# Kernel optimization log

Hardware: AMD Instinct MI355X
Metric: run time of the kernel (lower is better)

## Reference

```python
import jax, jax.numpy as jnp
import numpy as np
from jax import lax

B, DIM, H, W = 32, 64, 1, 8192
HEADS = 8
EPS_LN = 1e-5
EPS_NORM = 1e-12


def setup_inputs() -> dict:
    key = jax.random.key(0)
    ks = jax.random.split(key, 20)
    g = lambda i, shape, s=0.05: jax.random.normal(ks[i], shape, jnp.float32) * s
    return dict(
        x=jax.random.normal(ks[0], (B, DIM, H, W), jnp.float32),
        qkv_w=g(1, (3 * DIM, DIM)), qkv_b=g(2, (3 * DIM,)),
        dw_w=g(3, (3 * DIM, 1, 3, 3)), dw_b=g(4, (3 * DIM,)),
        proj_w=g(5, (DIM, DIM)), proj_b=g(6, (DIM,)),
        temperature=jnp.ones((HEADS, 1, 1), jnp.float32),
        sp_w=g(7, (DIM,)), sp_b=g(8, (1,)),
        up_w=g(9, (3,)), up_b=g(10, (3,)),
        c2_w=g(11, (1, 1, 2)), c2_b=g(11, (1,)), ln2_w=jnp.ones((W,), jnp.float32), ln2_b=jnp.zeros((W,), jnp.float32),
        c4_w=g(12, (1, 1, 4)), c4_b=g(13, (1,)), ln4_w=jnp.ones((W,), jnp.float32), ln4_b=jnp.zeros((W,), jnp.float32),
        c6_w=g(14, (1, 1, 6)), c6_b=g(15, (1,)), ln6_w=jnp.ones((W,), jnp.float32), ln6_b=jnp.zeros((W,), jnp.float32),
        mp_w=g(16, (DIM,)), mp_b=g(17, (DIM,)),
    )


def _mtl(xs, cw, cb, lw, lb):
    """Multiscale_Temporal_Layer: conv1d 'same' -> LayerNorm(W) -> ELU -> mean pool. xs: (b,1,w)."""
    k = cw.shape[-1]
    tot = k - 1
    lo = tot // 2  # torch 'same': extra pad goes to the right
    y = lax.conv_general_dilated(xs, cw, (1,), [(lo, tot - lo)],
                                 dimension_numbers=('NCH', 'OIH', 'NCH'))
    y = y + cb[None, :, None]
    mu = jnp.mean(y, -1, keepdims=True)
    var = jnp.mean((y - mu) ** 2, -1, keepdims=True)
    y = (y - mu) / jnp.sqrt(var + EPS_LN) * lw + lb
    y = jax.nn.elu(y)
    return jnp.mean(y, -1, keepdims=True)  # (b,1,1)


def _forward(x, qkv_w, qkv_b, dw_w, dw_b, proj_w, proj_b, temperature,
             sp_w, sp_b, up_w, up_b,
             c2_w, c2_b, ln2_w, ln2_b,
             c4_w, c4_b, ln4_w, ln4_b,
             c6_w, c6_b, ln6_w, ln6_b,
             mp_w, mp_b):
    b, c, h, w = x.shape
    hd = c // HEADS  # per-head channel dim
    # 1x1 conv qkv, then depthwise 3x3 conv
    qkv = jnp.einsum('oc,bchw->bohw', qkv_w, x) + qkv_b[None, :, None, None]
    qkv = lax.conv_general_dilated(qkv, dw_w, (1, 1), [(1, 1), (1, 1)],
                                   dimension_numbers=('NCHW', 'OIHW', 'NCHW'),
                                   feature_group_count=3 * c)
    qkv = qkv + dw_b[None, :, None, None]
    q, k, v = jnp.split(qkv, 3, axis=1)
    # Multiscale_Temporal_Attention on v: v is (b,c,1,w)
    xseq = (jnp.einsum('c,bcw->bw', sp_w, v[:, :, 0, :]) + sp_b)[:, None, :]  # (b,1,w)
    up = up_w[None, :, None] * xseq + up_b[None, :, None]  # (b,3,w)
    xx, yy, zz = up[:, 0:1], up[:, 1:2], up[:, 2:3]
    mout = (_mtl(xx, c2_w, c2_b, ln2_w, ln2_b) * xx
            + _mtl(yy, c4_w, c4_b, ln4_w, ln4_b) * yy
            + _mtl(zz, c6_w, c6_b, ln6_w, ln6_b) * zz)  # (b,1,w)
    v = mp_w[None, :, None] * mout + mp_b[None, :, None]  # (b,c,w) via 1x1 conv broadcast
    # channel (transposed) attention over n = h*w tokens
    n = h * w
    q = q.reshape(b, HEADS, hd, n)
    k = k.reshape(b, HEADS, hd, n)
    v = v.reshape(b, HEADS, hd, n)
    q = q / jnp.maximum(jnp.linalg.norm(q, axis=-1, keepdims=True), EPS_NORM)
    k = k / jnp.maximum(jnp.linalg.norm(k, axis=-1, keepdims=True), EPS_NORM)
    attn = jnp.einsum('bhcn,bhdn->bhcd', q, k) * temperature  # (b,heads,hd,hd)
    attn = jax.nn.softmax(attn, axis=-1)
    out = jnp.einsum('bhcd,bhdn->bhcn', attn, v).reshape(b, c, h, w)
    out = jnp.einsum('oc,bchw->bohw', proj_w, out) + proj_b[None, :, None, None]
    return out  # dropouts are identity in eval mode


def reference(x, qkv_w, qkv_b, dw_w, dw_b, proj_w, proj_b, temperature,
              sp_w, sp_b, up_w, up_b,
              c2_w, c2_b, ln2_w, ln2_b,
              c4_w, c4_b, ln4_w, ln4_b,
              c6_w, c6_b, ln6_w, ln6_b,
              mp_w, mp_b):
    return _forward(x, qkv_w, qkv_b, dw_w, dw_b, proj_w, proj_b, temperature,
                    sp_w, sp_b, up_w, up_b,
                    c2_w, c2_b, ln2_w, ln2_b,
                    c4_w, c4_b, ln4_w, ln4_b,
                    c6_w, c6_b, ln6_w, ln6_b,
                    mp_w, mp_b)
```

## Files before the change

### kernel.cpp

```cpp
#include <hip/hip_runtime.h>
#include <hip/hip_bf16.h>
#include <math.h>

#define Wd 8192
#define Bd 32

#define OFF_G    0
#define OFF_H    192
#define OFF_BASE 195
#define OFF_XSEQ 256
#define OFF_SXP  (OFF_XSEQ + Bd*Wd)
#define OFF_RX   (OFF_SXP + Bd*8*64)
#define OFF_T    (OFF_RX + Bd*8*12288)
#define OFF_VEC  (OFF_T + Bd*3*1152)
#define OFF_WM   (OFF_VEC + Bd*640)

typedef __attribute__((ext_vector_type(8))) short bf16x8;
typedef __attribute__((ext_vector_type(4))) float f32x4;

__device__ __forceinline__ unsigned short f2bf(float v) {
    return __builtin_bit_cast(unsigned short, __float2bfloat16(v));
}
__device__ __forceinline__ float bf2f(unsigned short h) {
    return __builtin_bit_cast(float, (unsigned)h << 16);
}

__global__ __launch_bounds__(256) void k0_setup(const float* __restrict__ qkv_w,
                         const float* __restrict__ qkv_b,
                         const float* __restrict__ dw_w, const float* __restrict__ dw_b,
                         const float* __restrict__ sp_w, const float* __restrict__ sp_b,
                         float* __restrict__ ws)
{
    __shared__ float sw[64*64];
    __shared__ float sdw[192];
    __shared__ float ssp[64], sqb[64], sdb[64];
    int tid = threadIdx.x;
    for (int i = tid; i < 4096; i += 256) sw[i] = qkv_w[128*64 + i];
    if (tid < 192) { int c = tid/3, j = tid - 3*c; sdw[tid] = dw_w[(128+c)*9 + 3 + j]; }
    if (tid < 64)  { ssp[tid] = sp_w[tid]; sqb[tid] = qkv_b[128+tid]; sdb[tid] = dw_b[128+tid]; }
    __syncthreads();
    if (tid < 192) {
        int j = tid >> 6, ch = tid & 63;
        float acc = 0.f;
        #pragma unroll 8
        for (int c = 0; c < 64; c++)
            acc += ssp[c] * sdw[c*3+j] * sw[c*64 + ch];
        ws[OFF_G + j*64 + ch] = acc;
    } else if (tid < 195) {
        int j = tid - 192;
        float h = 0.f;
        #pragma unroll 8
        for (int c = 0; c < 64; c++)
            h += ssp[c] * sdw[c*3+j] * sqb[c];
        ws[OFF_H + j] = h;
    } else if (tid == 195) {
        float base = sp_b[0];
        #pragma unroll 8
        for (int c = 0; c < 64; c++) base += ssp[c] * sdb[c];
        ws[OFF_BASE] = base;
    }
}

#define XSTR 152
#define XBYTES (64*XSTR*2)

__device__ __forceinline__ void loadpf(const float* __restrict__ xr, int wstart,
                                       int q, float4 pf[9]) {
    #pragma unroll
    for (int m = 0; m < 9; m++) {
        int gp = wstart - 8 + 36*q + 4*m;
        if (gp >= 0 && gp < Wd) pf[m] = *(const float4*)(xr + gp);
        else pf[m] = (float4){0.f,0.f,0.f,0.f};
    }
}
__device__ __forceinline__ float writepf(unsigned char* buf, int row, int q,
                                         const float4 pf[9]) {
    float ss = 0.f;
    #pragma unroll
    for (int m = 0; m < 9; m++) {
        int col0 = 36*q + 4*m;
        unsigned short h0 = f2bf(pf[m].x), h1 = f2bf(pf[m].y),
                       h2 = f2bf(pf[m].z), h3 = f2bf(pf[m].w);
        uint2 wv;
        wv.x = (unsigned)h0 | ((unsigned)h1 << 16);
        wv.y = (unsigned)h2 | ((unsigned)h3 << 16);
        *(uint2*)(buf + row*304 + col0*2) = wv;
        if (col0 >= 8 && col0 < 136)
            ss += (bf2f(h0) + bf2f(h1)) + (bf2f(h2) + bf2f(h3));
    }
    return ss;
}

__global__ __launch_bounds__(256) void kR(const float* __restrict__ x,
                                          float* __restrict__ ws)
{
    __shared__ __align__(16) unsigned char xb0[XBYTES];
    __shared__ __align__(16) unsigned char xb1[XBYTES];
    __shared__ float4 Gl[64];
    __shared__ float phib[3][132];
    __shared__ float sxb[64][4];

    const int tid = threadIdx.x, lane = tid & 63, wv = tid >> 6;
    const int g = lane >> 4, lr = lane & 15;
    const int chunk = blockIdx.x, b = blockIdx.y;
    const int w0 = chunk << 10;
    const int row = tid & 63, q = tid >> 6;
    const float* xr = x + ((size_t)b*64 + row)*Wd;

    if (tid < 64) Gl[tid] = (float4){ws[OFF_G+tid], ws[OFF_G+64+tid], ws[OFF_G+128+tid], 0.f};
    const float Hs0 = ws[OFF_H], Hs1 = ws[OFF_H+1], Hs2 = ws[OFF_H+2];
    const float base_ = ws[OFF_BASE];

    f32x4 a0[4], a1[4], a2[4];
    #pragma unroll
    for (int ct = 0; ct < 4; ct++) {
        a0[ct] = (f32x4){0,0,0,0}; a1[ct] = (f32x4){0,0,0,0}; a2[ct] = (f32x4){0,0,0,0};
    }
    float ssum = 0.f;
    float4 pf[9];

    loadpf(xr, w0, q, pf);
    ssum += writepf(xb0, row, q, pf);
    __syncthreads();

    for (int st = 0; st < 8; ++st) {
        const int p0 = w0 + (st << 7);
        unsigned char* bufc = (st & 1) ? xb1 : xb0;
        unsigned char* bufn = (st & 1) ? xb0 : xb1;

        if (st < 7) loadpf(xr, p0 + 128, q, pf);

        #pragma unroll
        for (int k = 0; k < 4; k++) {
            const unsigned char* ap = bufc + (16*wv + lr)*304 + 16 + 64*k + 16*g;
            bf16x8 A = *(const bf16x8*)ap;
            #pragma unroll
            for (int ct = 0; ct < 4; ct++) {
                const unsigned char* bp = bufc + (16*ct + lr)*304 + 16 + 64*k + 16*g;
                uint4 u = *(const uint4*)bp;
                unsigned u4 = *(const unsigned*)(bp + 16);
                uint4 v1 = { (u.x>>16)|(u.y<<16), (u.y>>16)|(u.z<<16),
                             (u.z>>16)|(u.w<<16), (u.w>>16)|(u4<<16) };
                uint4 v2 = { u.y, u.z, u.w, u4 };
                a0[ct] = __builtin_amdgcn_mfma_f32_16x16x32_bf16(A, __builtin_bit_cast(bf16x8,u),  a0[ct],0,0,0);
                a1[ct] = __builtin_amdgcn_mfma_f32_16x16x32_bf16(A, __builtin_bit_cast(bf16x8,v1), a1[ct],0,0,0);
                a2[ct] = __builtin_amdgcn_mfma_f32_16x16x32_bf16(A, __builtin_bit_cast(bf16x8,v2), a2[ct],0,0,0);
            }
        }
        if (tid < 130) {
            const unsigned short* xs = (const unsigned short*)bufc;
            float f0=0.f, f1=0.f, f2=0.f;
            int colw = 7 + tid;
            #pragma unroll 8
            for (int c = 0; c < 64; c++) {
                float xv = bf2f(xs[c*XSTR + colw]);
                float4 gv = Gl[c];
                f0 += gv.x*xv; f1 += gv.y*xv; f2 += gv.z*xv;
            }
            phib[0][tid]=f0; phib[1][tid]=f1; phib[2][tid]=f2;
        }
        __syncthreads();
        if (tid < 128) {
            int w = p0 + tid;
            float v = base_ + Hs0 + Hs1 + Hs2
                    + phib[0][tid] + phib[1][tid+1] + phib[2][tid+2];
            if (w == 0) v -= Hs0;
            if (w == Wd-1) v -= Hs2;
            ws[OFF_XSEQ + (size_t)b*Wd + w] = v;
        }
        if (st < 7) ssum += writepf(bufn, row, q, pf);
        __syncthreads();
    }

    {
        float* pb = ws + OFF_RX + (size_t)(b*8 + chunk)*12288;
        #pragma unroll
        for (int ct = 0; ct < 4; ct++) {
            #pragma unroll
            for (int r = 0; r < 4; r++) {
                int c = 16*wv + 4*g + r, cc = 16*ct + lr;
                pb[         c*64 + cc] = a0[ct][r];
                pb[4096  +  c*64 + cc] = a1[ct][r];
                pb[8192  +  c*64 + cc] = a2[ct][r];
            }
        }
    }
    sxb[row][q] = ssum;
    __syncthreads();
    if (tid < 64)
        ws[OFF_SXP + (size_t)(b*8 + chunk)*64 + tid] =
            (sxb[tid][0] + sxb[tid][1]) + (sxb[tid][2] + sxb[tid][3]);
}

#define KF_SW 0
#define KF_RX (128*68*4)
#define KF_NT (KF_RX + 64*68*4)
#define KF_SXR (KF_NT + 64*68*4)
#define KF_XC (KF_SXR + 64*4)
#define KF_BYTES (KF_XC + 256*4)

__device__ __forceinline__ float dot64p(const float* a, const float* b) {
    float s0=0.f,s1=0.f,s2=0.f,s3=0.f;
    #pragma unroll
    for (int k = 0; k < 64; k += 4) {
        float4 av = *(const float4*)(a+k), bv = *(const float4*)(b+k);
        s0 += av.x*bv.x; s1 += av.y*bv.y; s2 += av.z*bv.z; s3 += av.w*bv.w;
    }
    return (s0+s1)+(s2+s3);
}
__device__ __forceinline__ float blk_reduce_256(float v, float* sc) {
    #pragma unroll
    for (int off = 32; off > 0; off >>= 1) v += __shfl_down(v, off, 64);
    __syncthreads();
    if ((threadIdx.x & 63) == 0) sc[threadIdx.x >> 6] = v;
    __syncthreads();
    return sc[0] + sc[1] + sc[2] + sc[3];
}

__global__ __launch_bounds__(256) void kF(const float* __restrict__ x,
    const float* __restrict__ qkv_w,
    const float* __restrict__ up_w, const float* __restrict__ up_b,
    const float* __restrict__ c2_w, const float* __restrict__ c2_b,
    const float* __restrict__ ln2_w, const float* __restrict__ ln2_b,
    const float* __restrict__ c4_w, const float* __restrict__ c4_b,
    const float* __restrict__ ln4_w, const float* __restrict__ ln4_b,
    const float* __restrict__ c6_w, const float* __restrict__ c6_b,
    const float* __restrict__ ln6_w, const float* __restrict__ ln6_b,
    float* __restrict__ ws)
{
    __shared__ __align__(16) unsigned char sm[KF_BYTES];
    __shared__ float sc[4];
    const int tid = threadIdx.x, bx = blockIdx.x;

    if (bx < 96) {
        const int bb = bx / 3, d = bx - 3*bb;
        float* sW  = (float*)(sm + KF_SW);
        float* sRx = (float*)(sm + KF_RX);
        float* sNT = (float*)(sm + KF_NT);
        float* sxr = (float*)(sm + KF_SXR);
        float* xcol = (float*)(sm + KF_XC);

        #pragma unroll
        for (int k = 0; k < 8; k++) {
            int i4 = tid + 256*k;
            float4 v = ((const float4*)qkv_w)[i4];
            int r = i4 >> 4, c = (i4 & 15) << 2;
            *(float4*)(sW + r*68 + c) = v;
        }
        const float* rxp = ws + OFF_RX + (size_t)bb*8*12288 + d*4096;
        #pragma unroll
        for (int k = 0; k < 16; k++) {
            int idx = tid + 256*k;
            float s = 0.f;
            #pragma unroll
            for (int ch = 0; ch < 8; ch++) s += rxp[(size_t)ch*12288 + idx];
            sRx[(idx>>6)*68 + (idx&63)] = s;
        }
        if (d == 0) {
            if (tid < 64) {
                float s = 0.f;
                #pragma unroll
                for (int ch = 0; ch < 8; ch++) s += ws[OFF_SXP + (size_t)(bb*8+ch)*64 + tid];
                sxr[tid] = s;
            }
            {
                int c = tid & 63, v = tid >> 6;
                int colv = (v == 0) ? 0 : (v == 1) ? 1 : (v == 2) ? (Wd-2) : (Wd-1);
                xcol[v*64 + c] = x[((size_t)bb*64 + c)*Wd + colv];
            }
        }
        __syncthreads();
        if (d == 0 && tid < 128) {
            int r = tid;
            float Xi=0.f,x0=0.f,x1=0.f,xm2=0.f,xm1=0.f;
            #pragma unroll 8
            for (int c = 0; c < 64; c++) {
                float w = sW[r*68+c];
                Xi += w*sxr[c]; x0 += w*xcol[c]; x1 += w*xcol[64+c];
                xm2 += w*xcol[128+c]; xm1 += w*xcol[192+c];
            }
            float* vp = ws + OFF_VEC + bb*640;
            vp[r] = Xi; vp[128+r] = x0; vp[256+r] = x1; vp[384+r] = xm2; vp[512+r] = xm1;
        }
        {
            int ro = tid >> 4, co = tid & 15;
            float acc[4][4] = {};
            for (int k = 0; k < 64; k += 4) {
                float4 av[4], bv[4];
                #pragma unroll
                for (int i = 0; i < 4; i++) av[i] = *(const float4*)(sRx + (4*ro+i)*68 + k);
                #pragma unroll
                for (int j = 0; j < 4; j++) bv[j] = *(const float4*)(sW + (64+4*co+j)*68 + k);
                #pragma unroll
                for (int i = 0; i < 4; i++)
                    #pragma unroll
                    for (int j = 0; j < 4; j++)
                        acc[i][j] += av[i].x*bv[j].x + av[i].y*bv[j].y
                                   + av[i].z*bv[j].z + av[i].w*bv[j].w;
            }
            __syncthreads();
            #pragma unroll
            for (int i = 0; i < 4; i++)
                #pragma unroll
                for (int j = 0; j < 4; j++)
                    sNT[(4*co+j)*68 + 4*ro+i] = acc[i][j];
        }
        __syncthreads();
        float* Tp = ws + OFF_T + (size_t)(bb*3 + d)*1152;
        for (int e = tid; e < 512; e += 256) {
            int t = e >> 3, u = ((e>>6)<<3) + (e&7);
            Tp[e] = dot64p(sW + t*68, sNT + u*68);
        }
        if (tid < 64) Tp[1088 + tid] = dot64p(sW + (64+tid)*68, sNT + tid*68);
        __syncthreads();
        {
            int ro = tid >> 4, co = tid & 15;
            float acc[4][4] = {};
            for (int k = 0; k < 64; k += 4) {
                float4 av[4], bv[4];
                #pragma unroll
                for (int i = 0; i < 4; i++) av[i] = *(const float4*)(sRx + (4*ro+i)*68 + k);
                #pragma unroll
                for (int j = 0; j < 4; j++) bv[j] = *(const float4*)(sW + (4*co+j)*68 + k);
                #pragma unroll
                for (int i = 0; i < 4; i++)
                    #pragma unroll
                    for (int j = 0; j < 4; j++)
                        acc[i][j] += av[i].x*bv[j].x + av[i].y*bv[j].y
                                   + av[i].z*bv[j].z + av[i].w*bv[j].w;
            }
            __syncthreads();
            #pragma unroll
            for (int i = 0; i < 4; i++)
                #pragma unroll
                for (int j = 0; j < 4; j++)
                    sNT[(4*co+j)*68 + 4*ro+i] = acc[i][j];
        }
        __syncthreads();
        for (int e = tid; e < 512; e += 256) {
            int t = e >> 3, u = ((e>>6)<<3) + (e&7);
            Tp[512 + e] = dot64p(sW + (64+u)*68, sNT + t*68);
        }
        if (tid < 64) Tp[1024 + tid] = dot64p(sW + tid*68, sNT + tid*68);
        return;
    }

    int t2 = bx - 96;
    int br = t2 >> 5, b = t2 & 31;
    float* ys = (float*)sm;
    const float *cw, *lw, *lb; float cb; int K, lo;
    if (br == 0)      { cw = c2_w; cb = c2_b[0]; lw = ln2_w; lb = ln2_b; K = 2; lo = 0; }
    else if (br == 1) { cw = c4_w; cb = c4_b[0]; lw = ln4_w; lb = ln4_b; K = 4; lo = 1; }
    else              { cw = c6_w; cb = c6_b[0]; lw = ln6_w; lb = ln6_b; K = 6; lo = 2; }
    float uw = up_w[br], ub = up_b[br];
    const float* xr = ws + OFF_XSEQ + (size_t)b*Wd;

    float s = 0.f, s2 = 0.f;
    for (int w = tid; w < Wd; w += 256) {
        float y = cb;
        for (int m = 0; m < K; m++) {
            int p = w + m - lo;
            if (p >= 0 && p < Wd) y += cw[m] * (uw*xr[p] + ub);
        }
        ys[w] = y; s += y; s2 += y*y;
    }
    float mu = blk_reduce_256(s, sc) * (1.f/Wd);
    __syncthreads();
    float Ey2 = blk_reduce_256(s2, sc) * (1.f/Wd);
    float var = fmaxf(Ey2 - mu*mu, 0.f);
    float inv = 1.f / sqrtf(var + 1e-5f);
    float se = 0.f;
    for (int w = tid; w < Wd; w += 256) {
        float tt = (ys[w]-mu)*inv*lw[w] + lb[w];
        se += (tt > 0.f) ? tt : expm1f(tt);
    }
    float m = blk_reduce_256(se, sc) * (1.f/Wd);
    if (tid == 0) ws[OFF_WM + b*3 + br] = m;
}

__global__ __launch_bounds__(256) void k5_out(const float* __restrict__ ws,
    const float* __restrict__ qkv_b, const float* __restrict__ dw_w,
    const float* __restrict__ dw_b, const float* __restrict__ temperature,
    const float* __restrict__ mp_w, const float* __restrict__ mp_b,
    const float* __restrict__ up_w, const float* __restrict__ up_b,
    const float* __restrict__ proj_w, const float* __restrict__ proj_b,
    float* __restrict__ out)
{
    __shared__ float sT3[3][1152];
    __shared__ float vec[5][128];
    __shared__ float qb_[128], tb_[128], tp_[128][3];
    __shared__ float Sq[512], dgq[64], dgk[64];
    __shared__ float snk[64], sal[64], sbe[64], sE[64], sF[64];
    __shared__ float red[64][8];
    const int tid = threadIdx.x;
    const int chunk = blockIdx.x, b = blockIdx.y;

    for (int i = tid; i < 3456; i += 256) ((float*)sT3)[i] = ws[OFF_T + (size_t)b*3456 + i];
    for (int i = tid; i < 640; i += 256) ((float*)vec)[i] = ws[OFF_VEC + b*640 + i];
    if (tid < 128) {
        qb_[tid] = qkv_b[tid]; tb_[tid] = dw_b[tid];
        tp_[tid][0] = dw_w[tid*9+3]; tp_[tid][1] = dw_w[tid*9+4]; tp_[tid][2] = dw_w[tid*9+5];
    }
    __syncthreads();

    for (int ee = tid; ee < 640; ee += 256) {
        int r, s; float Tpv[3], Tmv[3];
        if (ee < 512) {
            r = ee >> 3; s = 64 + ((ee>>6)<<3) + (ee&7);
            #pragma unroll
            for (int d = 0; d < 3; d++) { Tpv[d] = sT3[d][ee]; Tmv[d] = sT3[d][512+ee]; }
        } else if (ee < 576) {
            r = s = ee - 512;
            #pragma unroll
            for (int d = 0; d < 3; d++) { Tpv[d] = Tmv[d] = sT3[d][1024 + r]; }
        } else {
            int u = ee - 576; r = s = 64 + u;
            #pragma unroll
            for (int d = 0; d < 3; d++) { Tpv[d] = Tmv[d] = sT3[d][1088 + u]; }
        }
        float Xr = vec[0][r], Xs = vec[0][s];
        float x0r = vec[1][r], x0s = vec[1][s];
        float x1r = vec[2][r], x1s = vec[2][s];
        float xm2r = vec[3][r], xm2s = vec[3][s];
        float xm1r = vec[4][r], xm1s = vec[4][s];
        float qr = qb_[r], qs = qb_[s];
        float C5[5];
        #pragma unroll
        for (int dd = 0; dd < 3; dd++) {
            float head_s = (dd>=1 ? x0s : 0.f) + (dd>=2 ? x1s : 0.f);
            float tail_r = (dd>=1 ? xm1r : 0.f) + (dd>=2 ? xm2r : 0.f);
            C5[2+dd] = Tpv[dd] + qr*(Xs - head_s) + qs*(Xr - tail_r) + (8192.f - dd)*qr*qs;
            float head_r = (dd>=1 ? x0r : 0.f) + (dd>=2 ? x1r : 0.f);
            float tail_s = (dd>=1 ? xm1s : 0.f) + (dd>=2 ? xm2s : 0.f);
            C5[2-dd] = Tmv[dd] + qs*(Xr - head_r) + qr*(Xs - tail_s) + (8192.f - dd)*qr*qs;
        }
        float y0r = x0r + qr, y0s = x0s + qs;
        float ym1r = xm1r + qr, ym1s = xm1s + qs;
        float Yr = Xr + 8192.f*qr, Ys = Xs + 8192.f*qs;
        float tbr = tb_[r], tbs = tb_[s];
        float G = 8192.f * tbr * tbs;
        float sumr = 0.f, sums = 0.f;
        #pragma unroll
        for (int i = 0; i < 3; i++) {
            sumr += tp_[r][i] * (Yr - (i==0 ? ym1r : 0.f) - (i==2 ? y0r : 0.f));
            sums += tp_[s][i] * (Ys - (i==0 ? ym1s : 0.f) - (i==2 ? y0s : 0.f));
        }
        G += tbr * sums + tbs * sumr;
        #pragma unroll
        for (int i = 0; i < 3; i++)
            #pragma unroll
            for (int j = 0; j < 3; j++) {
                float P = C5[2 + j - i];
                if (i == 2 && j == 2) P -= y0r * y0s;
                if (i == 0 && j == 0) P -= ym1r * ym1s;
                G += tp_[r][i] * tp_[s][j] * P;
            }
        if (ee < 512) Sq[ee] = G;
        else if (ee < 576) dgq[ee-512] = G;
        else dgk[ee-576] = G;
    }
    __syncthreads();

    float nq = 0.f;
    if (tid < 64) {
        nq = fmaxf(sqrtf(fmaxf(dgq[tid], 0.f)), 1e-12f);
        snk[tid] = fmaxf(sqrtf(fmaxf(dgk[tid], 0.f)), 1e-12f);
    }
    __syncthreads();
    if (tid < 64) {
        int h = tid >> 3;
        float temp = temperature[h];
        float lg[8], mx = -1e30f;
        #pragma unroll
        for (int d = 0; d < 8; d++) {
            lg[d] = Sq[tid*8 + d] / (nq * snk[h*8 + d]) * temp;
            mx = fmaxf(mx, lg[d]);
        }
        float sum = 0.f;
        #pragma unroll
        for (int d = 0; d < 8; d++) { lg[d] = expf(lg[d] - mx); sum += lg[d]; }
        float a = 0.f, bb2 = 0.f;
        #pragma unroll
        for (int d = 0; d < 8; d++) {
            float at = lg[d] / sum;
            a   += at * mp_w[h*8 + d];
            bb2 += at * mp_b[h*8 + d];
        }
        sal[tid] = a; sbe[tid] = bb2;
    }
    __syncthreads();
    {
        float m2 = ws[OFF_WM + b*3], m4 = ws[OFF_WM + b*3 + 1], m6 = ws[OFF_WM + b*3 + 2];
        float A_ = m2*up_w[0] + m4*up_w[1] + m6*up_w[2];
        float C_ = m2*up_b[0] + m4*up_b[1] + m6*up_b[2];
        int o = tid & 63, q = tid >> 6;
        float pa = 0.f, pb2 = 0.f;
        #pragma unroll
        for (int k = 0; k < 16; k++) {
            int c = 16*q + k;
            float pw = proj_w[o*64 + c];
            pa += pw * sal[c]; pb2 += pw * sbe[c];
        }
        red[o][q] = pa; red[o][4+q] = pb2;
        __syncthreads();
        if (tid < 64) {
            float Pa = (red[tid][0]+red[tid][1]) + (red[tid][2]+red[tid][3]);
            float Pb = (red[tid][4]+red[tid][5]) + (red[tid][6]+red[tid][7]);
            sE[tid] = A_ * Pa;
            sF[tid] = C_ * Pa + Pb + proj_b[tid];
        }
    }
    __syncthreads();
    const float4* xs4 = (const float4*)(ws + OFF_XSEQ + (size_t)b*Wd);
    float4 xv = xs4[chunk*128 + (tid & 127)];
    int oh = tid >> 7;
    float4* ob = (float4*)out + (size_t)b*64*2048 + chunk*128 + (tid & 127);
    #pragma unroll 8
    for (int oo = 0; oo < 32; oo++) {
        int o = oh*32 + oo;
        float e = sE[o], f = sF[o];
        float4 rr = { e*xv.x + f, e*xv.y + f, e*xv.z + f, e*xv.w + f };
        ob[(size_t)o*2048] = rr;
    }
}

extern "C" void kernel_launch(void* const* d_in, const int* in_sizes, int n_in,
                              void* d_out, int out_size, void* d_ws, size_t ws_size,
                              hipStream_t stream) {
    const float* x      = (const float*)d_in[0];
    const float* qkv_w  = (const float*)d_in[1];
    const float* qkv_b  = (const float*)d_in[2];
    const float* dw_w   = (const float*)d_in[3];
    const float* dw_b   = (const float*)d_in[4];
    const float* proj_w = (const float*)d_in[5];
    const float* proj_b = (const float*)d_in[6];
    const float* temperature = (const float*)d_in[7];
    const float* sp_w   = (const float*)d_in[8];
    const float* sp_b   = (const float*)d_in[9];
    const float* up_w   = (const float*)d_in[10];
    const float* up_b   = (const float*)d_in[11];
    const float* c2_w   = (const float*)d_in[12];
    const float* c2_b   = (const float*)d_in[13];
    const float* ln2_w  = (const float*)d_in[14];
    const float* ln2_b  = (const float*)d_in[15];
    const float* c4_w   = (const float*)d_in[16];
    const float* c4_b   = (const float*)d_in[17];
    const float* ln4_w  = (const float*)d_in[18];
    const float* ln4_b  = (const float*)d_in[19];
    const float* c6_w   = (const float*)d_in[20];
    const float* c6_b   = (const float*)d_in[21];
    const float* ln6_w  = (const float*)d_in[22];
    const float* ln6_b  = (const float*)d_in[23];
    const float* mp_w   = (const float*)d_in[24];
    const float* mp_b   = (const float*)d_in[25];
    float* ws  = (float*)d_ws;
    float* out = (float*)d_out;

    k0_setup<<<1, 256, 0, stream>>>(qkv_w, qkv_b, dw_w, dw_b, sp_w, sp_b, ws);
    kR<<<dim3(8, 32), 256, 0, stream>>>(x, ws);
    kF<<<192, 256, 0, stream>>>(x, qkv_w, up_w, up_b,
        c2_w, c2_b, ln2_w, ln2_b, c4_w, c4_b, ln4_w, ln4_b, c6_w, c6_b, ln6_w, ln6_b,
        ws);
    k5_out<<<dim3(16, 32), 256, 0, stream>>>(ws, qkv_b, dw_w, dw_b, temperature,
        mp_w, mp_b, up_w, up_b, proj_w, proj_b, out);
}
```

Baseline: 129.1 us.

## Split kR into 16 chunks with wider swizzled LDS tiles and coalesced loads

```diff
diff --git a/kernel.cpp b/kernel.cpp
--- a/kernel.cpp
+++ b/kernel.cpp
@@ -4,14 +4,15 @@
 
 #define Wd 8192
 #define Bd 32
+#define NCH 16
 
 #define OFF_G    0
 #define OFF_H    192
 #define OFF_BASE 195
 #define OFF_XSEQ 256
 #define OFF_SXP  (OFF_XSEQ + Bd*Wd)
-#define OFF_RX   (OFF_SXP + Bd*8*64)
-#define OFF_T    (OFF_RX + Bd*8*12288)
+#define OFF_RX   (OFF_SXP + Bd*NCH*64)
+#define OFF_T    (OFF_RX + Bd*NCH*12288)
 #define OFF_VEC  (OFF_T + Bd*3*1152)
 #define OFF_WM   (OFF_VEC + Bd*640)
 
@@ -61,51 +62,57 @@
     }
 }
 
-#define XSTR 152
-#define XBYTES (64*XSTR*2)
-
-__device__ __forceinline__ void loadpf(const float* __restrict__ xr, int wstart,
-                                       int q, float4 pf[9]) {
+#define ROWB 576
+
+__device__ __forceinline__ int swzoff(int row, int gr) {
+    int s = (gr < 32) ? (gr ^ (row & 7)) : gr;
+    return row*ROWB + s*16;
+}
+
+__device__ __forceinline__ void loadsub(const float* __restrict__ xbase, int p0,
+                                        float4 pf[17]) {
     #pragma unroll
-    for (int m = 0; m < 9; m++) {
-        int gp = wstart - 8 + 36*q + 4*m;
-        if (gp >= 0 && gp < Wd) pf[m] = *(const float4*)(xr + gp);
-        else pf[m] = (float4){0.f,0.f,0.f,0.f};
-    }
-}
-__device__ __forceinline__ float writepf(unsigned char* buf, int row, int q,
-                                         const float4 pf[9]) {
-    float ss = 0.f;
+    for (int m = 0; m < 17; m++) {
+        int F = threadIdx.x + 256*m;
+        int row = F / 68, c4 = F - 68*row;
+        int p = p0 - 8 + 4*c4;
+        const float* src = xbase + (size_t)row*Wd + p;
+        if ((unsigned)p <= (unsigned)(Wd-4)) {
+            pf[m] = *(const float4*)src;
+        } else {
+            float4 v;
+            v.x = ((unsigned)(p  ) < (unsigned)Wd) ? src[0] : 0.f;
+            v.y = ((unsigned)(p+1) < (unsigned)Wd) ? src[1] : 0.f;
+            v.z = ((unsigned)(p+2) < (unsigned)Wd) ? src[2] : 0.f;
+            v.w = ((unsigned)(p+3) < (unsigned)Wd) ? src[3] : 0.f;
+            pf[m] = v;
+        }
+    }
+}
+__device__ __forceinline__ void writesub(unsigned char* xb, const float4 pf[17]) {
     #pragma unroll
-    for (int m = 0; m < 9; m++) {
-        int col0 = 36*q + 4*m;
-        unsigned short h0 = f2bf(pf[m].x), h1 = f2bf(pf[m].y),
-                       h2 = f2bf(pf[m].z), h3 = f2bf(pf[m].w);
+    for (int m = 0; m < 17; m++) {
+        int F = threadIdx.x + 256*m;
+        int row = F / 68, c4 = F - 68*row;
         uint2 wv;
-        wv.x = (unsigned)h0 | ((unsigned)h1 << 16);
-        wv.y = (unsigned)h2 | ((unsigned)h3 << 16);
-        *(uint2*)(buf + row*304 + col0*2) = wv;
-        if (col0 >= 8 && col0 < 136)
-            ss += (bf2f(h0) + bf2f(h1)) + (bf2f(h2) + bf2f(h3));
-    }
-    return ss;
+        wv.x = (unsigned)f2bf(pf[m].x) | ((unsigned)f2bf(pf[m].y) << 16);
+        wv.y = (unsigned)f2bf(pf[m].z) | ((unsigned)f2bf(pf[m].w) << 16);
+        *(uint2*)(xb + swzoff(row, c4 >> 1) + (c4 & 1)*8) = wv;
+    }
 }
 
 __global__ __launch_bounds__(256) void kR(const float* __restrict__ x,
                                           float* __restrict__ ws)
 {
-    __shared__ __align__(16) unsigned char xb0[XBYTES];
-    __shared__ __align__(16) unsigned char xb1[XBYTES];
+    __shared__ __align__(16) unsigned char xb[64*ROWB];
+    __shared__ float phib[3][260];
     __shared__ float4 Gl[64];
-    __shared__ float phib[3][132];
     __shared__ float sxb[64][4];
 
     const int tid = threadIdx.x, lane = tid & 63, wv = tid >> 6;
     const int g = lane >> 4, lr = lane & 15;
-    const int chunk = blockIdx.x, b = blockIdx.y;
-    const int w0 = chunk << 10;
-    const int row = tid & 63, q = tid >> 6;
-    const float* xr = x + ((size_t)b*64 + row)*Wd;
+    const int grp = blockIdx.x, b = blockIdx.y;
+    const float* xbase = x + (size_t)b*64*Wd;
 
     if (tid < 64) Gl[tid] = (float4){ws[OFF_G+tid], ws[OFF_G+64+tid], ws[OFF_G+128+tid], 0.f};
     const float Hs0 = ws[OFF_H], Hs1 = ws[OFF_H+1], Hs2 = ws[OFF_H+2];
@@ -116,29 +123,27 @@
     for (int ct = 0; ct < 4; ct++) {
         a0[ct] = (f32x4){0,0,0,0}; a1[ct] = (f32x4){0,0,0,0}; a2[ct] = (f32x4){0,0,0,0};
     }
-    float ssum = 0.f;
-    float4 pf[9];
-
-    loadpf(xr, w0, q, pf);
-    ssum += writepf(xb0, row, q, pf);
-    __syncthreads();
-
-    for (int st = 0; st < 8; ++st) {
-        const int p0 = w0 + (st << 7);
-        unsigned char* bufc = (st & 1) ? xb1 : xb0;
-        unsigned char* bufn = (st & 1) ? xb0 : xb1;
-
-        if (st < 7) loadpf(xr, p0 + 128, q, pf);
-
-        #pragma unroll
-        for (int k = 0; k < 4; k++) {
-            const unsigned char* ap = bufc + (16*wv + lr)*304 + 16 + 64*k + 16*g;
-            bf16x8 A = *(const bf16x8*)ap;
+    float rs = 0.f;
+    float4 pf[17];
+
+    loadsub(xbase, grp*512, pf);
+    writesub(xb, pf);
+    __syncthreads();
+
+    #pragma unroll
+    for (int s = 0; s < 2; s++) {
+        const int p0 = grp*512 + s*256;
+        if (s == 0) loadsub(xbase, p0 + 256, pf);
+
+        #pragma unroll
+        for (int ks = 0; ks < 8; ks++) {
+            int gr0 = 1 + 4*ks + g;
+            bf16x8 A = *(const bf16x8*)(xb + swzoff(16*wv + lr, gr0));
             #pragma unroll
             for (int ct = 0; ct < 4; ct++) {
-                const unsigned char* bp = bufc + (16*ct + lr)*304 + 16 + 64*k + 16*g;
-                uint4 u = *(const uint4*)bp;
-                unsigned u4 = *(const unsigned*)(bp + 16);
+                int rb = 16*ct + lr;
+                uint4 u = *(const uint4*)(xb + swzoff(rb, gr0));
+                unsigned u4 = *(const unsigned*)(xb + swzoff(rb, gr0 + 1));
                 uint4 v1 = { (u.x>>16)|(u.y<<16), (u.y>>16)|(u.z<<16),
                              (u.z>>16)|(u.w<<16), (u.w>>16)|(u4<<16) };
                 uint4 v2 = { u.y, u.z, u.w, u4 };
@@ -147,20 +152,33 @@
                 a2[ct] = __builtin_amdgcn_mfma_f32_16x16x32_bf16(A, __builtin_bit_cast(bf16x8,v2), a2[ct],0,0,0);
             }
         }
-        if (tid < 130) {
-            const unsigned short* xs = (const unsigned short*)bufc;
-            float f0=0.f, f1=0.f, f2=0.f;
-            int colw = 7 + tid;
+        for (int ci = tid; ci < 258; ci += 256) {
+            int col = 7 + ci;
+            int grc = col >> 3, off = (col & 7)*2;
+            float f0 = 0.f, f1 = 0.f, f2 = 0.f;
             #pragma unroll 8
             for (int c = 0; c < 64; c++) {
-                float xv = bf2f(xs[c*XSTR + colw]);
+                float xv = bf2f(*(const unsigned short*)(xb + swzoff(c, grc) + off));
                 float4 gv = Gl[c];
                 f0 += gv.x*xv; f1 += gv.y*xv; f2 += gv.z*xv;
             }
-            phib[0][tid]=f0; phib[1][tid]=f1; phib[2][tid]=f2;
-        }
-        __syncthreads();
-        if (tid < 128) {
+            phib[0][ci] = f0; phib[1][ci] = f1; phib[2][ci] = f2;
+        }
+        {
+            int row = tid & 63, q = tid >> 6;
+            float ssum = 0.f;
+            #pragma unroll
+            for (int i = 0; i < 8; i++) {
+                uint4 u = *(const uint4*)(xb + swzoff(row, 1 + 8*q + i));
+                ssum += (bf2f((unsigned short)u.x) + bf2f((unsigned short)(u.x>>16)))
+                      + (bf2f((unsigned short)u.y) + bf2f((unsigned short)(u.y>>16)))
+                      + (bf2f((unsigned short)u.z) + bf2f((unsigned short)(u.z>>16)))
+                      + (bf2f((unsigned short)u.w) + bf2f((unsigned short)(u.w>>16)));
+            }
+            rs += ssum;
+        }
+        __syncthreads();
+        {
             int w = p0 + tid;
             float v = base_ + Hs0 + Hs1 + Hs2
                     + phib[0][tid] + phib[1][tid+1] + phib[2][tid+2];
@@ -168,27 +186,33 @@
             if (w == Wd-1) v -= Hs2;
             ws[OFF_XSEQ + (size_t)b*Wd + w] = v;
         }
-        if (st < 7) ssum += writepf(bufn, row, q, pf);
-        __syncthreads();
+        __syncthreads();
+        if (s == 0) {
+            writesub(xb, pf);
+            __syncthreads();
+        }
     }
 
     {
-        float* pb = ws + OFF_RX + (size_t)(b*8 + chunk)*12288;
+        float* pb = ws + OFF_RX + (size_t)(b*NCH + grp)*12288;
         #pragma unroll
         for (int ct = 0; ct < 4; ct++) {
             #pragma unroll
             for (int r = 0; r < 4; r++) {
                 int c = 16*wv + 4*g + r, cc = 16*ct + lr;
-                pb[         c*64 + cc] = a0[ct][r];
-                pb[4096  +  c*64 + cc] = a1[ct][r];
-                pb[8192  +  c*64 + cc] = a2[ct][r];
-            }
-        }
-    }
-    sxb[row][q] = ssum;
+                pb[        c*64 + cc] = a0[ct][r];
+                pb[4096 +  c*64 + cc] = a1[ct][r];
+                pb[8192 +  c*64 + cc] = a2[ct][r];
+            }
+        }
+    }
+    {
+        int row = tid & 63, q = tid >> 6;
+        sxb[row][q] = rs;
+    }
     __syncthreads();
     if (tid < 64)
-        ws[OFF_SXP + (size_t)(b*8 + chunk)*64 + tid] =
+        ws[OFF_SXP + (size_t)(b*NCH + grp)*64 + tid] =
             (sxb[tid][0] + sxb[tid][1]) + (sxb[tid][2] + sxb[tid][3]);
 }
 
@@ -247,20 +271,20 @@
             int r = i4 >> 4, c = (i4 & 15) << 2;
             *(float4*)(sW + r*68 + c) = v;
         }
-        const float* rxp = ws + OFF_RX + (size_t)bb*8*12288 + d*4096;
+        const float* rxp = ws + OFF_RX + (size_t)bb*NCH*12288 + d*4096;
         #pragma unroll
         for (int k = 0; k < 16; k++) {
             int idx = tid + 256*k;
             float s = 0.f;
             #pragma unroll
-            for (int ch = 0; ch < 8; ch++) s += rxp[(size_t)ch*12288 + idx];
+            for (int ch = 0; ch < NCH; ch++) s += rxp[(size_t)ch*12288 + idx];
             sRx[(idx>>6)*68 + (idx&63)] = s;
         }
         if (d == 0) {
             if (tid < 64) {
                 float s = 0.f;
                 #pragma unroll
-                for (int ch = 0; ch < 8; ch++) s += ws[OFF_SXP + (size_t)(bb*8+ch)*64 + tid];
+                for (int ch = 0; ch < NCH; ch++) s += ws[OFF_SXP + (size_t)(bb*NCH+ch)*64 + tid];
                 sxr[tid] = s;
             }
             {
@@ -557,7 +581,7 @@
     float* out = (float*)d_out;
 
     k0_setup<<<1, 256, 0, stream>>>(qkv_w, qkv_b, dw_w, dw_b, sp_w, sp_b, ws);
-    kR<<<dim3(8, 32), 256, 0, stream>>>(x, ws);
+    kR<<<dim3(NCH, 32), 256, 0, stream>>>(x, ws);
     kF<<<192, 256, 0, stream>>>(x, qkv_w, up_w, up_b,
         c2_w, c2_b, ln2_w, ln2_b, c4_w, c4_b, ln4_w, ln4_b, c6_w, c6_b, ln6_w, ln6_b,
         ws);
```

Measured after the change: 121.4 us. 1.06x faster.
